# Performance work log

Hardware: AMD Instinct MI355X
Metric: run time of the kernel (lower is better)

The kernel has to match this reference:

```python
import jax, jax.numpy as jnp
import numpy as np


def _linear_interp(t, S):
    """1D linear interpolation along last axis, matching F.interpolate(mode='linear', align_corners=False).
    t: [B, C, L] -> [B, C, S]"""
    L = t.shape[-1]
    src = jnp.clip((jnp.arange(S, dtype=jnp.float32) + 0.5) * (L / S) - 0.5, 0.0, L - 1)
    i0 = jnp.floor(src).astype(jnp.int32)
    i1 = jnp.minimum(i0 + 1, L - 1)
    w = (src - i0.astype(jnp.float32)).astype(t.dtype)
    return t[..., i0] * (1.0 - w) + t[..., i1] * w


def setup_inputs() -> dict:
    key = jax.random.key(0)
    k1, k2, k3, k4 = jax.random.split(key, 4)
    B, C, H, W, L, D = 32, 768, 32, 32, 77, 512
    return {
        "img_feat": jax.random.normal(k1, (B, C, H, W), dtype=jnp.float32),
        "text_feat": jax.random.normal(k2, (B, L, D), dtype=jnp.float32),
        "W_txt": jax.random.normal(k3, (D, C), dtype=jnp.float32) / np.float32(np.sqrt(D)),
        "gamma": jax.random.normal(k4, (1,), dtype=jnp.float32) * 0.1,
    }


def reference(img_feat, text_feat, W_txt, gamma):
    B, C, H, W = img_feat.shape
    S = H * W
    q = img_feat.reshape(B, C, S)                          # [B,C,S]
    # Linear(D->C, bias=False) then transpose(1,2): [B,L,D] -> [B,C,L]
    t = jnp.einsum('bld,dc->bcl', text_feat, W_txt)
    t = _linear_interp(t, S)                               # [B,C,S]
    scale = S ** (-0.5)
    # attn = bmm(q [B,C,S], t^T [B,S,C]) * scale -> [B,C,C] channel attention
    attn = jax.nn.softmax(jnp.einsum('bis,bjs->bij', q, t) * scale, axis=-1)
    out = q + gamma * jnp.einsum('bij,bjs->bis', attn, t)  # gamma-gated residual
    return out.reshape(B, C, H, W)
```

## Files before the change

### kernel.cpp

```cpp
#include <hip/hip_runtime.h>

#define BB 32
#define CC 768
#define SS 1024
#define LLn 77
#define DD 512
#define LP 80
#define LP2 96
#define QBS 264
#define WREG 8448

#define RATIO 0.0751953125f

#define CVT_TXT_BLOCKS (BB * LP * DD / 4 / 256)
#define CVT_W_BLOCKS ((CC / 32) * (DD / 32))
#define AB_BLOCKS (4 * 5 * 8 * 64 * 8 / 4 / 256)
#define TG_BLOCKS (BB * 5 * 4)

typedef short bf16x8 __attribute__((ext_vector_type(8)));
typedef float f32x4 __attribute__((ext_vector_type(4)));
typedef unsigned short u16;

#define MFMA __builtin_amdgcn_mfma_f32_16x16x32_bf16

__device__ __forceinline__ float bf2f(unsigned int h16) {
    unsigned int u = h16 << 16;
    float f; __builtin_memcpy(&f, &u, 4); return f;
}
__device__ __forceinline__ u16 f2bf(float f) {
    unsigned int u; __builtin_memcpy(&u, &f, 4);
    u += 0x7fffu + ((u >> 16) & 1u);
    return (u16)(u >> 16);
}

__global__ __launch_bounds__(256) void k_cvt(const float* __restrict__ text,
                                             const float* __restrict__ Wt,
                                             u16* __restrict__ At,
                                             u16* __restrict__ Wb,
                                             u16* __restrict__ Abf) {
    __shared__ float tile[32 * 33];
    const int bx = blockIdx.x;
    const int tid = threadIdx.x;
    if (bx < CVT_TXT_BLOCKS) {
        int j = bx * 256 + tid;
        int row80 = j >> 7, col4 = (j & 127) << 2;
        int b = row80 / LP, l = row80 - b * LP;
        u16 o[4] = {0, 0, 0, 0};
        if (l < LLn) {
            float4 v = *reinterpret_cast<const float4*>(&text[((size_t)b * LLn + l) * DD + col4]);
            o[0] = f2bf(v.x); o[1] = f2bf(v.y); o[2] = f2bf(v.z); o[3] = f2bf(v.w);
        }
        *reinterpret_cast<uint2*>(&At[(size_t)row80 * DD + col4]) = *reinterpret_cast<uint2*>(o);
    } else if (bx < CVT_TXT_BLOCKS + CVT_W_BLOCKS) {
        const int bw = bx - CVT_TXT_BLOCKS;
        const int c0 = (bw % (CC / 32)) * 32, d0 = (bw / (CC / 32)) * 32;
        const int tx = tid & 31, ty = tid >> 5;
#pragma unroll
        for (int k = 0; k < 4; ++k) {
            int d = ty + k * 8;
            tile[d * 33 + tx] = Wt[(size_t)(d0 + d) * CC + c0 + tx];
        }
        __syncthreads();
#pragma unroll
        for (int k = 0; k < 4; ++k) {
            int c = ty + k * 8;
            Wb[(size_t)(c0 + c) * DD + d0 + tx] = f2bf(tile[tx * 33 + c]);
        }
    } else {
        int g = (bx - CVT_TXT_BLOCKS - CVT_W_BLOCKS) * 1024 + tid * 4;
        int e0   = g & 7;
        int lane = (g >> 3) & 63;
        int kk   = (g >> 9) & 7;
        int nt   = (g >> 12) % 5;
        int w    = g / 20480;
        int l    = nt * 16 + (lane & 15);
        int sb   = w * 256 + kk * 32 + ((lane >> 4) << 3) + e0;
        float fl = (float)l;
        u16 o[4];
#pragma unroll
        for (int k = 0; k < 4; ++k) {
            float src = fmaf((float)(sb + k) + 0.5f, RATIO, -0.5f);
            src = fminf(fmaxf(src, 0.f), 76.f);
            o[k] = f2bf(fmaxf(0.f, 1.f - fabsf(src - fl)) * 0.03125f);
        }
        *reinterpret_cast<uint2*>(&Abf[g]) = *reinterpret_cast<uint2*>(o);
    }
}

__global__ __launch_bounds__(256) void k_tgemm(const u16* __restrict__ At,
                                               const u16* __restrict__ Wb,
                                               u16* __restrict__ tc,
                                               u16* __restrict__ tlc) {
    const int bx = blockIdx.x;
    const int tid = threadIdx.x;
    const int cg = bx / 160, mt = bx % 160;
    const int b = mt / 5, tile = mt % 5;
    const int l0 = tile * 16;
    const int w = tid >> 6, lane = tid & 63;
    const int lm = lane & 15, lg = lane >> 4;
    const int c0 = cg * 192 + w * 48;

    f32x4 acc[3];
#pragma unroll
    for (int nt = 0; nt < 3; ++nt) acc[nt] = (f32x4){0.f, 0.f, 0.f, 0.f};

    const u16* ap = At + ((size_t)b * LP + l0 + lm) * DD + lg * 8;
    const u16* bp = Wb + (size_t)(c0 + lm) * DD + lg * 8;
#pragma unroll 4
    for (int ks = 0; ks < 16; ++ks) {
        bf16x8 aq = *reinterpret_cast<const bf16x8*>(ap + ks * 32);
#pragma unroll
        for (int nt = 0; nt < 3; ++nt) {
            bf16x8 bv = *reinterpret_cast<const bf16x8*>(bp + (size_t)nt * 16 * DD + ks * 32);
            acc[nt] = MFMA(aq, bv, acc[nt], 0, 0, 0);
        }
    }

    const int lq = l0 + lg * 4;
#pragma unroll
    for (int nt = 0; nt < 3; ++nt) {
        int c = c0 + nt * 16 + lm;
        u16 pk[4];
#pragma unroll
        for (int r = 0; r < 4; ++r) pk[r] = f2bf(acc[nt][r]);
        uint2 pv; __builtin_memcpy(&pv, pk, 8);
        *reinterpret_cast<uint2*>(&tc[((size_t)b * CC + c) * LP2 + lq]) = pv;
#pragma unroll
        for (int r = 0; r < 4; ++r)
            tlc[((size_t)b * LP + lq + r) * CC + c] = pk[r];
    }
    if (tile == 4 && lg == 0) {
        uint4 z = {0u, 0u, 0u, 0u};
#pragma unroll
        for (int nt = 0; nt < 3; ++nt) {
            int c = c0 + nt * 16 + lm;
            *reinterpret_cast<uint4*>(&tc[((size_t)b * CC + c) * LP2 + 80]) = z;
            *reinterpret_cast<uint4*>(&tc[((size_t)b * CC + c) * LP2 + 88]) = z;
        }
    }
}

__global__ __launch_bounds__(256, 3) void k_fused(const u16* __restrict__ tc,
                                                  const u16* __restrict__ tlc,
                                                  const u16* __restrict__ Abf,
                                                  const float* __restrict__ q,
                                                  const float* __restrict__ gamma,
                                                  float* __restrict__ out) {
    __shared__ __align__(16) char un[4 * WREG];
    __shared__ __align__(16) char sh2[5120];
    __shared__ float pmax[64];
    __shared__ float psum[64];

    const int id = blockIdx.x;
    const int o = id >> 3;
    const int b = (id & 7) * 4 + o / 48;
    const int iBase = (o % 48) * 16;

    const int tid = threadIdx.x;
    const int w = tid >> 6, lane = tid & 63;
    const int lm = lane & 15, lg = lane >> 4;
    const float g = gamma[0];

    const size_t qBase = ((size_t)b * CC + iBase) * SS + (size_t)(tid << 2);
    const int s0 = tid << 2;
    uint2 qpk[16];
#pragma unroll
    for (int r = 0; r < 16; ++r) {
        f32x4 v = *reinterpret_cast<const f32x4*>(&q[qBase + (size_t)r * SS]);
        u16 pk[4] = {f2bf(v[0]), f2bf(v[1]), f2bf(v[2]), f2bf(v[3])};
        __builtin_memcpy(&qpk[r], pk, 8);
    }
    u16* qbuf = (u16*)(un + w * WREG);
#pragma unroll
    for (int r = 0; r < 16; ++r)
        *reinterpret_cast<uint2*>(&qbuf[r * QBS + lane * 4]) = qpk[r];

    f32x4 aqh[5];
#pragma unroll
    for (int nt = 0; nt < 5; ++nt) aqh[nt] = (f32x4){0.f, 0.f, 0.f, 0.f};
    const u16* abw = Abf + ((size_t)(w * 5) << 12) + (lane << 3);
#pragma unroll
    for (int kk = 0; kk < 8; ++kk) {
        bf16x8 av = *reinterpret_cast<const bf16x8*>(&qbuf[lm * QBS + kk * 32 + lg * 8]);
#pragma unroll
        for (int nt = 0; nt < 5; ++nt) {
            bf16x8 bv = *reinterpret_cast<const bf16x8*>(abw + (((nt << 3) + kk) << 9));
            aqh[nt] = MFMA(av, bv, aqh[nt], 0, 0, 0);
        }
    }
    {
        float* qp = (float*)(un + w * WREG);
#pragma unroll
        for (int nt = 0; nt < 5; ++nt) {
#pragma unroll
            for (int r = 0; r < 4; ++r)
                qp[(lg * 4 + r) * 80 + nt * 16 + lm] = aqh[nt][r];
        }
    }
    __syncthreads();

    u16* qh_bf = (u16*)sh2;
#pragma unroll
    for (int k = 0; k < 5; ++k) {
        int e = tid + (k << 8);
        int row = e / 80, l = e - row * 80;
        float v = ((float*)(un))[row * 80 + l]
                + ((float*)(un + WREG))[row * 80 + l]
                + ((float*)(un + 2 * WREG))[row * 80 + l]
                + ((float*)(un + 3 * WREG))[row * 80 + l];
        qh_bf[row * 96 + l] = f2bf(v);
    }
    if (tid < 16 * 16) qh_bf[(tid >> 4) * 96 + 80 + (tid & 15)] = 0;
    __syncthreads();

    bf16x8 aq0 = *reinterpret_cast<const bf16x8*>(&qh_bf[lm * 96 + lg * 8]);
    bf16x8 aq1 = *reinterpret_cast<const bf16x8*>(&qh_bf[lm * 96 + 32 + lg * 8]);
    bf16x8 aq2 = *reinterpret_cast<const bf16x8*>(&qh_bf[lm * 96 + 64 + lg * 8]);

    f32x4 acc[12];
#pragma unroll
    for (int t = 0; t < 12; ++t) acc[t] = (f32x4){0.f, 0.f, 0.f, 0.f};

    const u16* tcb = tc + ((size_t)b * CC + w * 192 + lm) * LP2 + lg * 8;
#pragma unroll
    for (int t = 0; t < 12; ++t) {
        const u16* p = tcb + (size_t)t * 16 * LP2;
        bf16x8 b0 = *reinterpret_cast<const bf16x8*>(p);
        bf16x8 b1 = *reinterpret_cast<const bf16x8*>(p + 32);
        bf16x8 b2 = *reinterpret_cast<const bf16x8*>(p + 64);
        acc[t] = MFMA(aq0, b0, acc[t], 0, 0, 0);
        acc[t] = MFMA(aq1, b1, acc[t], 0, 0, 0);
        acc[t] = MFMA(aq2, b2, acc[t], 0, 0, 0);
    }

    float m[4];
#pragma unroll
    for (int r = 0; r < 4; ++r) {
        float mm = acc[0][r];
#pragma unroll
        for (int t = 1; t < 12; ++t) mm = fmaxf(mm, acc[t][r]);
#pragma unroll
        for (int off = 8; off >= 1; off >>= 1) mm = fmaxf(mm, __shfl_xor(mm, off));
        m[r] = mm;
    }
    if (lm == 0) {
#pragma unroll
        for (int r = 0; r < 4; ++r) pmax[w * 16 + lg * 4 + r] = m[r];
    }
    __syncthreads();
    float gm[4];
#pragma unroll
    for (int r = 0; r < 4; ++r) {
        int row = lg * 4 + r;
        gm[r] = fmaxf(fmaxf(pmax[row], pmax[16 + row]), fmaxf(pmax[32 + row], pmax[48 + row]));
    }
    float s[4] = {0.f, 0.f, 0.f, 0.f};
#pragma unroll
    for (int t = 0; t < 12; ++t) {
#pragma unroll
        for (int r = 0; r < 4; ++r) {
            float e = __expf(acc[t][r] - gm[r]);
            acc[t][r] = e;
            s[r] += e;
        }
    }
#pragma unroll
    for (int r = 0; r < 4; ++r) {
#pragma unroll
        for (int off = 8; off >= 1; off >>= 1) s[r] += __shfl_xor(s[r], off);
    }
    if (lm == 0) {
#pragma unroll
        for (int r = 0; r < 4; ++r) psum[w * 16 + lg * 4 + r] = s[r];
    }

    u16* P = (u16*)(un + w * WREG);
#pragma unroll
    for (int t = 0; t < 12; ++t) {
#pragma unroll
        for (int r = 0; r < 4; ++r)
            P[(lg * 4 + r) * 200 + t * 16 + lm] = f2bf(acc[t][r]);
    }

    f32x4 u[5];
#pragma unroll
    for (int nt = 0; nt < 5; ++nt) u[nt] = (f32x4){0.f, 0.f, 0.f, 0.f};
    const u16* tb = tlc + ((size_t)b * LP + lm) * CC + w * 192 + lg * 8;
#pragma unroll
    for (int ks = 0; ks < 6; ++ks) {
        bf16x8 pa = *reinterpret_cast<const bf16x8*>(&P[lm * 200 + ks * 32 + lg * 8]);
#pragma unroll
        for (int nt = 0; nt < 5; ++nt) {
            bf16x8 bv = *reinterpret_cast<const bf16x8*>(tb + (size_t)nt * 16 * CC + ks * 32);
            u[nt] = MFMA(pa, bv, u[nt], 0, 0, 0);
        }
    }

    float* up = (float*)(un + w * WREG);
#pragma unroll
    for (int nt = 0; nt < 5; ++nt) {
#pragma unroll
        for (int r = 0; r < 4; ++r)
            up[(lg * 4 + r) * 81 + nt * 16 + lm] = u[nt][r];
    }
    __syncthreads();
    float* us = (float*)sh2;
#pragma unroll
    for (int k = 0; k < 5; ++k) {
        int idx = tid + (k << 8);
        int row = idx / LP, l = idx - row * LP;
        float v = ((float*)(un))[row * 81 + l]
                + ((float*)(un + WREG))[row * 81 + l]
                + ((float*)(un + 2 * WREG))[row * 81 + l]
                + ((float*)(un + 3 * WREG))[row * 81 + l];
        float denom = psum[row] + psum[16 + row] + psum[32 + row] + psum[48 + row];
        us[row * LP + l] = v / denom;
    }
    __syncthreads();

    float wgt[4]; int i0k[4], i1x[4];
#pragma unroll
    for (int k = 0; k < 4; ++k) {
        float src = fmaf((float)(s0 + k) + 0.5f, RATIO, -0.5f);
        src = fminf(fmaxf(src, 0.f), 76.f);
        i0k[k] = (int)src;
        wgt[k] = src - (float)i0k[k];
        i1x[k] = (i0k[k] < 76) ? i0k[k] + 1 : 76;
    }
#pragma unroll
    for (int r = 0; r < 16; ++r) {
        const float* ur = &us[r * LP];
        uint2 qq = qpk[r];
        float qf[4] = {bf2f(qq.x & 0xffffu), bf2f(qq.x >> 16),
                       bf2f(qq.y & 0xffffu), bf2f(qq.y >> 16)};
        f32x4 ov;
#pragma unroll
        for (int k = 0; k < 4; ++k) {
            float uv = fmaf(1.f - wgt[k], ur[i0k[k]], wgt[k] * ur[i1x[k]]);
            ov[k] = qf[k] + g * uv;
        }
        __builtin_nontemporal_store(ov, reinterpret_cast<f32x4*>(&out[qBase + (size_t)r * SS]));
    }
}

extern "C" void kernel_launch(void* const* d_in, const int* in_sizes, int n_in,
                              void* d_out, int out_size, void* d_ws, size_t ws_size,
                              hipStream_t stream) {
    const float* img   = (const float*)d_in[0];
    const float* text  = (const float*)d_in[1];
    const float* Wt    = (const float*)d_in[2];
    const float* gamma = (const float*)d_in[3];
    float* out = (float*)d_out;
    char* ws = (char*)d_ws;
    u16*   tc_bf  = (u16*)(ws);
    u16*   tlc_bf = (u16*)(ws + 4718592);
    u16*   At_bf  = (u16*)(ws + 8650752);
    u16*   Wb_bf  = (u16*)(ws + 11272192);
    u16*   Abf_bf = (u16*)(ws + 12058624);

    k_cvt<<<dim3(CVT_TXT_BLOCKS + CVT_W_BLOCKS + AB_BLOCKS), 256, 0, stream>>>(
        text, Wt, At_bf, Wb_bf, Abf_bf);
    k_tgemm<<<dim3(TG_BLOCKS), 256, 0, stream>>>(At_bf, Wb_bf, tc_bf, tlc_bf);
    k_fused<<<dim3(48 * BB), 256, 0, stream>>>(tc_bf, tlc_bf, Abf_bf, img, gamma, out);
}
```

Baseline: 97.70 us.

## Split fused attention block across eight waves instead of four

The fused kernel moves from 256 to 512 threads per block. Each wave now owns 128 spatial positions and 96 channels instead of 256 and 192. The interpolation matrix layout in the convert kernel is rearranged to match, and the cross-wave reductions now sum eight partials. The aim is more waves in flight per CU to hide latency on the q loads and tc/tlc reads. The cost is narrower global accesses (2-float loads and stores), more LDS reduction work and larger barrier groups.

```diff
diff --git a/kernel.cpp b/kernel.cpp
--- a/kernel.cpp
+++ b/kernel.cpp
@@ -7,19 +7,20 @@
 #define DD 512
 #define LP 80
 #define LP2 96
-#define QBS 264
-#define WREG 8448
+#define WREG2 5184
 
 #define RATIO 0.0751953125f
 
 #define CVT_TXT_BLOCKS (BB * LP * DD / 4 / 256)
 #define CVT_W_BLOCKS ((CC / 32) * (DD / 32))
-#define AB_BLOCKS (4 * 5 * 8 * 64 * 8 / 4 / 256)
+#define AB_BLOCKS (8 * 5 * 4 * 64 * 8 / 4 / 256)
 #define TG_BLOCKS (BB * 5 * 4)
 
 typedef short bf16x8 __attribute__((ext_vector_type(8)));
 typedef float f32x4 __attribute__((ext_vector_type(4)));
+typedef float f32x2 __attribute__((ext_vector_type(2)));
 typedef unsigned short u16;
+typedef unsigned int u32;
 
 #define MFMA __builtin_amdgcn_mfma_f32_16x16x32_bf16
 
@@ -70,11 +71,12 @@
         int g = (bx - CVT_TXT_BLOCKS - CVT_W_BLOCKS) * 1024 + tid * 4;
         int e0   = g & 7;
         int lane = (g >> 3) & 63;
-        int kk   = (g >> 9) & 7;
-        int nt   = (g >> 12) % 5;
-        int w    = g / 20480;
+        int kk   = (g >> 9) & 3;
+        int wn   = g >> 11;
+        int nt   = wn % 5;
+        int wv   = wn / 5;
         int l    = nt * 16 + (lane & 15);
-        int sb   = w * 256 + kk * 32 + ((lane >> 4) << 3) + e0;
+        int sb   = wv * 128 + kk * 32 + ((lane >> 4) << 3) + e0;
         float fl = (float)l;
         u16 o[4];
 #pragma unroll
@@ -140,16 +142,16 @@
     }
 }
 
-__global__ __launch_bounds__(256, 3) void k_fused(const u16* __restrict__ tc,
+__global__ __launch_bounds__(512, 4) void k_fused(const u16* __restrict__ tc,
                                                   const u16* __restrict__ tlc,
                                                   const u16* __restrict__ Abf,
                                                   const float* __restrict__ q,
                                                   const float* __restrict__ gamma,
                                                   float* __restrict__ out) {
-    __shared__ __align__(16) char un[4 * WREG];
+    __shared__ __align__(16) char un[8 * WREG2];
     __shared__ __align__(16) char sh2[5120];
-    __shared__ float pmax[64];
-    __shared__ float psum[64];
+    __shared__ float pmax[128];
+    __shared__ float psum[128];
 
     const int id = blockIdx.x;
     const int o = id >> 3;
@@ -157,39 +159,38 @@
     const int iBase = (o % 48) * 16;
 
     const int tid = threadIdx.x;
-    const int w = tid >> 6, lane = tid & 63;
+    const int wv = tid >> 6, lane = tid & 63;
     const int lm = lane & 15, lg = lane >> 4;
     const float g = gamma[0];
 
-    const size_t qBase = ((size_t)b * CC + iBase) * SS + (size_t)(tid << 2);
-    const int s0 = tid << 2;
-    uint2 qpk[16];
+    const int c0 = wv * 128 + lane * 2;
+    const size_t qRow = ((size_t)b * CC + iBase) * SS + c0;
+    u32 qpk[16];
 #pragma unroll
     for (int r = 0; r < 16; ++r) {
-        f32x4 v = *reinterpret_cast<const f32x4*>(&q[qBase + (size_t)r * SS]);
-        u16 pk[4] = {f2bf(v[0]), f2bf(v[1]), f2bf(v[2]), f2bf(v[3])};
-        __builtin_memcpy(&qpk[r], pk, 8);
-    }
-    u16* qbuf = (u16*)(un + w * WREG);
+        f32x2 v = *reinterpret_cast<const f32x2*>(&q[qRow + (size_t)r * SS]);
+        qpk[r] = (u32)f2bf(v[0]) | ((u32)f2bf(v[1]) << 16);
+    }
+    u16* qbuf = (u16*)(un + wv * WREG2);
 #pragma unroll
     for (int r = 0; r < 16; ++r)
-        *reinterpret_cast<uint2*>(&qbuf[r * QBS + lane * 4]) = qpk[r];
+        *reinterpret_cast<u32*>(&qbuf[r * 136 + lane * 2]) = qpk[r];
 
     f32x4 aqh[5];
 #pragma unroll
     for (int nt = 0; nt < 5; ++nt) aqh[nt] = (f32x4){0.f, 0.f, 0.f, 0.f};
-    const u16* abw = Abf + ((size_t)(w * 5) << 12) + (lane << 3);
-#pragma unroll
-    for (int kk = 0; kk < 8; ++kk) {
-        bf16x8 av = *reinterpret_cast<const bf16x8*>(&qbuf[lm * QBS + kk * 32 + lg * 8]);
+    const u16* abw = Abf + (size_t)wv * 10240 + lane * 8;
+#pragma unroll
+    for (int kk = 0; kk < 4; ++kk) {
+        bf16x8 av = *reinterpret_cast<const bf16x8*>(&qbuf[lm * 136 + kk * 32 + lg * 8]);
 #pragma unroll
         for (int nt = 0; nt < 5; ++nt) {
-            bf16x8 bv = *reinterpret_cast<const bf16x8*>(abw + (((nt << 3) + kk) << 9));
+            bf16x8 bv = *reinterpret_cast<const bf16x8*>(abw + ((nt * 4 + kk) << 9));
             aqh[nt] = MFMA(av, bv, aqh[nt], 0, 0, 0);
         }
     }
     {
-        float* qp = (float*)(un + w * WREG);
+        float* qp = (float*)(un + wv * WREG2);
 #pragma unroll
         for (int nt = 0; nt < 5; ++nt) {
 #pragma unroll
@@ -201,29 +202,30 @@
 
     u16* qh_bf = (u16*)sh2;
 #pragma unroll
-    for (int k = 0; k < 5; ++k) {
-        int e = tid + (k << 8);
-        int row = e / 80, l = e - row * 80;
-        float v = ((float*)(un))[row * 80 + l]
-                + ((float*)(un + WREG))[row * 80 + l]
-                + ((float*)(un + 2 * WREG))[row * 80 + l]
-                + ((float*)(un + 3 * WREG))[row * 80 + l];
-        qh_bf[row * 96 + l] = f2bf(v);
-    }
-    if (tid < 16 * 16) qh_bf[(tid >> 4) * 96 + 80 + (tid & 15)] = 0;
+    for (int k = 0; k < 3; ++k) {
+        int e = tid + (k << 9);
+        if (e < 1280) {
+            int row = e / 80, l = e - row * 80;
+            float v = 0.f;
+#pragma unroll
+            for (int i = 0; i < 8; ++i) v += ((float*)(un + i * WREG2))[row * 80 + l];
+            qh_bf[row * 96 + l] = f2bf(v);
+        }
+    }
+    if (tid < 256) qh_bf[(tid >> 4) * 96 + 80 + (tid & 15)] = 0;
     __syncthreads();
 
     bf16x8 aq0 = *reinterpret_cast<const bf16x8*>(&qh_bf[lm * 96 + lg * 8]);
     bf16x8 aq1 = *reinterpret_cast<const bf16x8*>(&qh_bf[lm * 96 + 32 + lg * 8]);
     bf16x8 aq2 = *reinterpret_cast<const bf16x8*>(&qh_bf[lm * 96 + 64 + lg * 8]);
 
-    f32x4 acc[12];
-#pragma unroll
-    for (int t = 0; t < 12; ++t) acc[t] = (f32x4){0.f, 0.f, 0.f, 0.f};
-
-    const u16* tcb = tc + ((size_t)b * CC + w * 192 + lm) * LP2 + lg * 8;
-#pragma unroll
-    for (int t = 0; t < 12; ++t) {
+    f32x4 acc[6];
+#pragma unroll
+    for (int t = 0; t < 6; ++t) acc[t] = (f32x4){0.f, 0.f, 0.f, 0.f};
+
+    const u16* tcb = tc + ((size_t)b * CC + wv * 96 + lm) * LP2 + lg * 8;
+#pragma unroll
+    for (int t = 0; t < 6; ++t) {
         const u16* p = tcb + (size_t)t * 16 * LP2;
         bf16x8 b0 = *reinterpret_cast<const bf16x8*>(p);
         bf16x8 b1 = *reinterpret_cast<const bf16x8*>(p + 32);
@@ -238,25 +240,29 @@
     for (int r = 0; r < 4; ++r) {
         float mm = acc[0][r];
 #pragma unroll
-        for (int t = 1; t < 12; ++t) mm = fmaxf(mm, acc[t][r]);
+        for (int t = 1; t < 6; ++t) mm = fmaxf(mm, acc[t][r]);
 #pragma unroll
         for (int off = 8; off >= 1; off >>= 1) mm = fmaxf(mm, __shfl_xor(mm, off));
         m[r] = mm;
     }
     if (lm == 0) {
 #pragma unroll
-        for (int r = 0; r < 4; ++r) pmax[w * 16 + lg * 4 + r] = m[r];
+        for (int r = 0; r < 4; ++r) pmax[wv * 16 + lg * 4 + r] = m[r];
     }
     __syncthreads();
     float gm[4];
 #pragma unroll
     for (int r = 0; r < 4; ++r) {
         int row = lg * 4 + r;
-        gm[r] = fmaxf(fmaxf(pmax[row], pmax[16 + row]), fmaxf(pmax[32 + row], pmax[48 + row]));
+        float a01 = fmaxf(pmax[row], pmax[16 + row]);
+        float a23 = fmaxf(pmax[32 + row], pmax[48 + row]);
+        float a45 = fmaxf(pmax[64 + row], pmax[80 + row]);
+        float a67 = fmaxf(pmax[96 + row], pmax[112 + row]);
+        gm[r] = fmaxf(fmaxf(a01, a23), fmaxf(a45, a67));
     }
     float s[4] = {0.f, 0.f, 0.f, 0.f};
 #pragma unroll
-    for (int t = 0; t < 12; ++t) {
+    for (int t = 0; t < 6; ++t) {
 #pragma unroll
         for (int r = 0; r < 4; ++r) {
             float e = __expf(acc[t][r] - gm[r]);
@@ -271,24 +277,24 @@
     }
     if (lm == 0) {
 #pragma unroll
-        for (int r = 0; r < 4; ++r) psum[w * 16 + lg * 4 + r] = s[r];
-    }
-
-    u16* P = (u16*)(un + w * WREG);
-#pragma unroll
-    for (int t = 0; t < 12; ++t) {
+        for (int r = 0; r < 4; ++r) psum[wv * 16 + lg * 4 + r] = s[r];
+    }
+
+    u16* P = (u16*)(un + wv * WREG2);
+#pragma unroll
+    for (int t = 0; t < 6; ++t) {
 #pragma unroll
         for (int r = 0; r < 4; ++r)
-            P[(lg * 4 + r) * 200 + t * 16 + lm] = f2bf(acc[t][r]);
+            P[(lg * 4 + r) * 104 + t * 16 + lm] = f2bf(acc[t][r]);
     }
 
     f32x4 u[5];
 #pragma unroll
     for (int nt = 0; nt < 5; ++nt) u[nt] = (f32x4){0.f, 0.f, 0.f, 0.f};
-    const u16* tb = tlc + ((size_t)b * LP + lm) * CC + w * 192 + lg * 8;
-#pragma unroll
-    for (int ks = 0; ks < 6; ++ks) {
-        bf16x8 pa = *reinterpret_cast<const bf16x8*>(&P[lm * 200 + ks * 32 + lg * 8]);
+    const u16* tb = tlc + ((size_t)b * LP + lm) * CC + wv * 96 + lg * 8;
+#pragma unroll
+    for (int ks = 0; ks < 3; ++ks) {
+        bf16x8 pa = *reinterpret_cast<const bf16x8*>(&P[lm * 104 + ks * 32 + lg * 8]);
 #pragma unroll
         for (int nt = 0; nt < 5; ++nt) {
             bf16x8 bv = *reinterpret_cast<const bf16x8*>(tb + (size_t)nt * 16 * CC + ks * 32);
@@ -296,7 +302,7 @@
         }
     }
 
-    float* up = (float*)(un + w * WREG);
+    float* up = (float*)(un + wv * WREG2);
 #pragma unroll
     for (int nt = 0; nt < 5; ++nt) {
 #pragma unroll
@@ -306,40 +312,37 @@
     __syncthreads();
     float* us = (float*)sh2;
 #pragma unroll
-    for (int k = 0; k < 5; ++k) {
-        int idx = tid + (k << 8);
-        int row = idx / LP, l = idx - row * LP;
-        float v = ((float*)(un))[row * 81 + l]
-                + ((float*)(un + WREG))[row * 81 + l]
-                + ((float*)(un + 2 * WREG))[row * 81 + l]
-                + ((float*)(un + 3 * WREG))[row * 81 + l];
-        float denom = psum[row] + psum[16 + row] + psum[32 + row] + psum[48 + row];
-        us[row * LP + l] = v / denom;
-    }
-    __syncthreads();
-
-    float wgt[4]; int i0k[4], i1x[4];
-#pragma unroll
-    for (int k = 0; k < 4; ++k) {
-        float src = fmaf((float)(s0 + k) + 0.5f, RATIO, -0.5f);
-        src = fminf(fmaxf(src, 0.f), 76.f);
-        i0k[k] = (int)src;
-        wgt[k] = src - (float)i0k[k];
-        i1x[k] = (i0k[k] < 76) ? i0k[k] + 1 : 76;
-    }
+    for (int k = 0; k < 3; ++k) {
+        int e = tid + (k << 9);
+        if (e < 1280) {
+            int row = e / 80, l = e - row * 80;
+            float v = 0.f;
+#pragma unroll
+            for (int i = 0; i < 8; ++i) v += ((float*)(un + i * WREG2))[row * 81 + l];
+            float denom = 0.f;
+#pragma unroll
+            for (int i = 0; i < 8; ++i) denom += psum[i * 16 + row];
+            us[row * 80 + l] = v / denom;
+        }
+    }
+    __syncthreads();
+
+    float srcA = fminf(fmaxf(fmaf((float)c0 + 0.5f, RATIO, -0.5f), 0.f), 76.f);
+    float srcB = fminf(fmaxf(fmaf((float)c0 + 1.5f, RATIO, -0.5f), 0.f), 76.f);
+    int i0a = (int)srcA, i0b = (int)srcB;
+    float wa = srcA - (float)i0a, wb = srcB - (float)i0b;
+    int i1a = (i0a < 76) ? i0a + 1 : 76;
+    int i1b = (i0b < 76) ? i0b + 1 : 76;
 #pragma unroll
     for (int r = 0; r < 16; ++r) {
-        const float* ur = &us[r * LP];
-        uint2 qq = qpk[r];
-        float qf[4] = {bf2f(qq.x & 0xffffu), bf2f(qq.x >> 16),
-                       bf2f(qq.y & 0xffffu), bf2f(qq.y >> 16)};
-        f32x4 ov;
-#pragma unroll
-        for (int k = 0; k < 4; ++k) {
-            float uv = fmaf(1.f - wgt[k], ur[i0k[k]], wgt[k] * ur[i1x[k]]);
-            ov[k] = qf[k] + g * uv;
-        }
-        __builtin_nontemporal_store(ov, reinterpret_cast<f32x4*>(&out[qBase + (size_t)r * SS]));
+        const float* ur = &us[r * 80];
+        float ua = fmaf(1.f - wa, ur[i0a], wa * ur[i1a]);
+        float ub = fmaf(1.f - wb, ur[i0b], wb * ur[i1b]);
+        u32 qq = qpk[r];
+        f32x2 ov;
+        ov[0] = bf2f(qq & 0xffffu) + g * ua;
+        ov[1] = bf2f(qq >> 16) + g * ub;
+        __builtin_nontemporal_store(ov, reinterpret_cast<f32x2*>(&out[qRow + (size_t)r * SS]));
     }
 }
 
@@ -361,5 +364,5 @@
     k_cvt<<<dim3(CVT_TXT_BLOCKS + CVT_W_BLOCKS + AB_BLOCKS), 256, 0, stream>>>(
         text, Wt, At_bf, Wb_bf, Abf_bf);
     k_tgemm<<<dim3(TG_BLOCKS), 256, 0, stream>>>(At_bf, Wb_bf, tc_bf, tlc_bf);
-    k_fused<<<dim3(48 * BB), 256, 0, stream>>>(tc_bf, tlc_bf, Abf_bf, img, gamma, out);
-}
+    k_fused<<<dim3(48 * BB), 512, 0, stream>>>(tc_bf, tlc_bf, Abf_bf, img, gamma, out);
+}
```

New measurement: 101.8 us. 4.2% more time.

## Split q-projection into the text GEMM kernel and reload q in fp32 for output

Applied to the files above, without the earlier changes.

The q·A interpolation projection (qh) moves out of the fused attention kernel into a combined middle kernel of 512-thread blocks that also runs the text GEMM. qh is written to global memory in bf16. The attention kernel then only reads qh, runs softmax and the second GEMM, and re-reads q in fp32 for the residual instead of keeping bf16 copies. The aim is to raise occupancy and overlap the two middle-stage workloads, and the fp32 residual also improves accuracy. In exchange q is read from HBM twice and qh takes an extra global round trip.

```diff
diff --git a/kernel.cpp b/kernel.cpp
--- a/kernel.cpp
+++ b/kernel.cpp
@@ -7,19 +7,21 @@
 #define DD 512
 #define LP 80
 #define LP2 96
-#define QBS 264
-#define WREG 8448
+#define WREG2 5184
 
 #define RATIO 0.0751953125f
 
 #define CVT_TXT_BLOCKS (BB * LP * DD / 4 / 256)
 #define CVT_W_BLOCKS ((CC / 32) * (DD / 32))
-#define AB_BLOCKS (4 * 5 * 8 * 64 * 8 / 4 / 256)
-#define TG_BLOCKS (BB * 5 * 4)
+#define AB_BLOCKS (8 * 5 * 4 * 64 * 8 / 4 / 256)
+#define QH_BLOCKS (48 * BB)
+#define TG2_BLOCKS (BB * 5 * 2)
 
 typedef short bf16x8 __attribute__((ext_vector_type(8)));
 typedef float f32x4 __attribute__((ext_vector_type(4)));
+typedef float f32x2 __attribute__((ext_vector_type(2)));
 typedef unsigned short u16;
+typedef unsigned int u32;
 
 #define MFMA __builtin_amdgcn_mfma_f32_16x16x32_bf16
 
@@ -70,11 +72,12 @@
         int g = (bx - CVT_TXT_BLOCKS - CVT_W_BLOCKS) * 1024 + tid * 4;
         int e0   = g & 7;
         int lane = (g >> 3) & 63;
-        int kk   = (g >> 9) & 7;
-        int nt   = (g >> 12) % 5;
-        int w    = g / 20480;
+        int kk   = (g >> 9) & 3;
+        int wn   = g >> 11;
+        int nt   = wn % 5;
+        int wv   = wn / 5;
         int l    = nt * 16 + (lane & 15);
-        int sb   = w * 256 + kk * 32 + ((lane >> 4) << 3) + e0;
+        int sb   = wv * 128 + kk * 32 + ((lane >> 4) << 3) + e0;
         float fl = (float)l;
         u16 o[4];
 #pragma unroll
@@ -87,135 +90,146 @@
     }
 }
 
-__global__ __launch_bounds__(256) void k_tgemm(const u16* __restrict__ At,
-                                               const u16* __restrict__ Wb,
-                                               u16* __restrict__ tc,
-                                               u16* __restrict__ tlc) {
+__global__ __launch_bounds__(512, 2) void k_mid2(const float* __restrict__ q,
+                                                 const u16* __restrict__ Abf,
+                                                 const u16* __restrict__ At,
+                                                 const u16* __restrict__ Wb,
+                                                 u16* __restrict__ qh,
+                                                 u16* __restrict__ tc,
+                                                 u16* __restrict__ tlc) {
+    __shared__ __align__(16) char un[8 * WREG2];
     const int bx = blockIdx.x;
     const int tid = threadIdx.x;
-    const int cg = bx / 160, mt = bx % 160;
-    const int b = mt / 5, tile = mt % 5;
-    const int l0 = tile * 16;
-    const int w = tid >> 6, lane = tid & 63;
+    const int wv = tid >> 6, lane = tid & 63;
     const int lm = lane & 15, lg = lane >> 4;
-    const int c0 = cg * 192 + w * 48;
-
-    f32x4 acc[3];
-#pragma unroll
-    for (int nt = 0; nt < 3; ++nt) acc[nt] = (f32x4){0.f, 0.f, 0.f, 0.f};
-
-    const u16* ap = At + ((size_t)b * LP + l0 + lm) * DD + lg * 8;
-    const u16* bp = Wb + (size_t)(c0 + lm) * DD + lg * 8;
+
+    if (bx < QH_BLOCKS) {
+        const int o = bx >> 3;
+        const int b = (bx & 7) * 4 + o / 48;
+        const int iBase = (o % 48) * 16;
+
+        const int c0 = wv * 128 + lane * 2;
+        const size_t qRow = ((size_t)b * CC + iBase) * SS + c0;
+        u32 qpk[16];
+#pragma unroll
+        for (int r = 0; r < 16; ++r) {
+            f32x2 v = *reinterpret_cast<const f32x2*>(&q[qRow + (size_t)r * SS]);
+            qpk[r] = (u32)f2bf(v[0]) | ((u32)f2bf(v[1]) << 16);
+        }
+        u16* qbuf = (u16*)(un + wv * WREG2);
+#pragma unroll
+        for (int r = 0; r < 16; ++r)
+            *reinterpret_cast<u32*>(&qbuf[r * 136 + lane * 2]) = qpk[r];
+
+        f32x4 aqh[5];
+#pragma unroll
+        for (int nt = 0; nt < 5; ++nt) aqh[nt] = (f32x4){0.f, 0.f, 0.f, 0.f};
+        const u16* abw = Abf + (size_t)wv * 10240 + lane * 8;
+#pragma unroll
+        for (int kk = 0; kk < 4; ++kk) {
+            bf16x8 av = *reinterpret_cast<const bf16x8*>(&qbuf[lm * 136 + kk * 32 + lg * 8]);
+#pragma unroll
+            for (int nt = 0; nt < 5; ++nt) {
+                bf16x8 bv = *reinterpret_cast<const bf16x8*>(abw + ((nt * 4 + kk) << 9));
+                aqh[nt] = MFMA(av, bv, aqh[nt], 0, 0, 0);
+            }
+        }
+        {
+            float* qp = (float*)(un + wv * WREG2);
+#pragma unroll
+            for (int nt = 0; nt < 5; ++nt) {
+#pragma unroll
+                for (int r = 0; r < 4; ++r)
+                    qp[(lg * 4 + r) * 80 + nt * 16 + lm] = aqh[nt][r];
+            }
+        }
+        __syncthreads();
+
+        for (int e2 = tid; e2 < 16 * 48; e2 += 512) {
+            int row = e2 / 48, j = e2 - row * 48;
+            int l0 = 2 * j;
+            float v0 = 0.f, v1 = 0.f;
+            if (l0 < 80) {
+#pragma unroll
+                for (int i = 0; i < 8; ++i) v0 += ((float*)(un + i * WREG2))[row * 80 + l0];
+#pragma unroll
+                for (int i = 0; i < 8; ++i) v1 += ((float*)(un + i * WREG2))[row * 80 + l0 + 1];
+            }
+            u32 pk = (u32)f2bf(v0) | ((u32)f2bf(v1) << 16);
+            *reinterpret_cast<u32*>(&qh[((size_t)b * CC + iBase + row) * LP2 + l0]) = pk;
+        }
+    } else {
+        const int bt = bx - QH_BLOCKS;
+        const int cg = bt / 160, mt = bt % 160;
+        const int b = mt / 5, tile = mt % 5;
+        const int l0 = tile * 16;
+        const int c0 = cg * 384 + wv * 48;
+
+        f32x4 acc[3];
+#pragma unroll
+        for (int nt = 0; nt < 3; ++nt) acc[nt] = (f32x4){0.f, 0.f, 0.f, 0.f};
+
+        const u16* ap = At + ((size_t)b * LP + l0 + lm) * DD + lg * 8;
+        const u16* bp = Wb + (size_t)(c0 + lm) * DD + lg * 8;
 #pragma unroll 4
-    for (int ks = 0; ks < 16; ++ks) {
-        bf16x8 aq = *reinterpret_cast<const bf16x8*>(ap + ks * 32);
-#pragma unroll
-        for (int nt = 0; nt < 3; ++nt) {
-            bf16x8 bv = *reinterpret_cast<const bf16x8*>(bp + (size_t)nt * 16 * DD + ks * 32);
-            acc[nt] = MFMA(aq, bv, acc[nt], 0, 0, 0);
-        }
-    }
-
-    const int lq = l0 + lg * 4;
-#pragma unroll
-    for (int nt = 0; nt < 3; ++nt) {
-        int c = c0 + nt * 16 + lm;
-        u16 pk[4];
-#pragma unroll
-        for (int r = 0; r < 4; ++r) pk[r] = f2bf(acc[nt][r]);
-        uint2 pv; __builtin_memcpy(&pv, pk, 8);
-        *reinterpret_cast<uint2*>(&tc[((size_t)b * CC + c) * LP2 + lq]) = pv;
-#pragma unroll
-        for (int r = 0; r < 4; ++r)
-            tlc[((size_t)b * LP + lq + r) * CC + c] = pk[r];
-    }
-    if (tile == 4 && lg == 0) {
-        uint4 z = {0u, 0u, 0u, 0u};
+        for (int ks = 0; ks < 16; ++ks) {
+            bf16x8 aq = *reinterpret_cast<const bf16x8*>(ap + ks * 32);
+#pragma unroll
+            for (int nt = 0; nt < 3; ++nt) {
+                bf16x8 bv = *reinterpret_cast<const bf16x8*>(bp + (size_t)nt * 16 * DD + ks * 32);
+                acc[nt] = MFMA(aq, bv, acc[nt], 0, 0, 0);
+            }
+        }
+
+        const int lq = l0 + lg * 4;
 #pragma unroll
         for (int nt = 0; nt < 3; ++nt) {
             int c = c0 + nt * 16 + lm;
-            *reinterpret_cast<uint4*>(&tc[((size_t)b * CC + c) * LP2 + 80]) = z;
-            *reinterpret_cast<uint4*>(&tc[((size_t)b * CC + c) * LP2 + 88]) = z;
-        }
-    }
-}
-
-__global__ __launch_bounds__(256, 3) void k_fused(const u16* __restrict__ tc,
-                                                  const u16* __restrict__ tlc,
-                                                  const u16* __restrict__ Abf,
-                                                  const float* __restrict__ q,
-                                                  const float* __restrict__ gamma,
-                                                  float* __restrict__ out) {
-    __shared__ __align__(16) char un[4 * WREG];
-    __shared__ __align__(16) char sh2[5120];
-    __shared__ float pmax[64];
-    __shared__ float psum[64];
+            u16 pk[4];
+#pragma unroll
+            for (int r = 0; r < 4; ++r) pk[r] = f2bf(acc[nt][r]);
+            uint2 pv; __builtin_memcpy(&pv, pk, 8);
+            *reinterpret_cast<uint2*>(&tc[((size_t)b * CC + c) * LP2 + lq]) = pv;
+#pragma unroll
+            for (int r = 0; r < 4; ++r)
+                tlc[((size_t)b * LP + lq + r) * CC + c] = pk[r];
+        }
+        if (tile == 4 && lg == 0) {
+            uint4 z = {0u, 0u, 0u, 0u};
+#pragma unroll
+            for (int nt = 0; nt < 3; ++nt) {
+                int c = c0 + nt * 16 + lm;
+                *reinterpret_cast<uint4*>(&tc[((size_t)b * CC + c) * LP2 + 80]) = z;
+                *reinterpret_cast<uint4*>(&tc[((size_t)b * CC + c) * LP2 + 88]) = z;
+            }
+        }
+    }
+}
+
+__global__ __launch_bounds__(256, 2) void k_attn_out(const u16* __restrict__ qh,
+                                                     const u16* __restrict__ tc,
+                                                     const u16* __restrict__ tlc,
+                                                     const float* __restrict__ q,
+                                                     const float* __restrict__ gamma,
+                                                     float* __restrict__ out) {
+    __shared__ float pmax[4][16];
+    __shared__ float psum[4][16];
+    __shared__ float us[16 * 80];
+    __shared__ __align__(16) char pbuf[4][6400];
 
     const int id = blockIdx.x;
     const int o = id >> 3;
     const int b = (id & 7) * 4 + o / 48;
     const int iBase = (o % 48) * 16;
-
     const int tid = threadIdx.x;
     const int w = tid >> 6, lane = tid & 63;
     const int lm = lane & 15, lg = lane >> 4;
     const float g = gamma[0];
 
-    const size_t qBase = ((size_t)b * CC + iBase) * SS + (size_t)(tid << 2);
-    const int s0 = tid << 2;
-    uint2 qpk[16];
-#pragma unroll
-    for (int r = 0; r < 16; ++r) {
-        f32x4 v = *reinterpret_cast<const f32x4*>(&q[qBase + (size_t)r * SS]);
-        u16 pk[4] = {f2bf(v[0]), f2bf(v[1]), f2bf(v[2]), f2bf(v[3])};
-        __builtin_memcpy(&qpk[r], pk, 8);
-    }
-    u16* qbuf = (u16*)(un + w * WREG);
-#pragma unroll
-    for (int r = 0; r < 16; ++r)
-        *reinterpret_cast<uint2*>(&qbuf[r * QBS + lane * 4]) = qpk[r];
-
-    f32x4 aqh[5];
-#pragma unroll
-    for (int nt = 0; nt < 5; ++nt) aqh[nt] = (f32x4){0.f, 0.f, 0.f, 0.f};
-    const u16* abw = Abf + ((size_t)(w * 5) << 12) + (lane << 3);
-#pragma unroll
-    for (int kk = 0; kk < 8; ++kk) {
-        bf16x8 av = *reinterpret_cast<const bf16x8*>(&qbuf[lm * QBS + kk * 32 + lg * 8]);
-#pragma unroll
-        for (int nt = 0; nt < 5; ++nt) {
-            bf16x8 bv = *reinterpret_cast<const bf16x8*>(abw + (((nt << 3) + kk) << 9));
-            aqh[nt] = MFMA(av, bv, aqh[nt], 0, 0, 0);
-        }
-    }
-    {
-        float* qp = (float*)(un + w * WREG);
-#pragma unroll
-        for (int nt = 0; nt < 5; ++nt) {
-#pragma unroll
-            for (int r = 0; r < 4; ++r)
-                qp[(lg * 4 + r) * 80 + nt * 16 + lm] = aqh[nt][r];
-        }
-    }
-    __syncthreads();
-
-    u16* qh_bf = (u16*)sh2;
-#pragma unroll
-    for (int k = 0; k < 5; ++k) {
-        int e = tid + (k << 8);
-        int row = e / 80, l = e - row * 80;
-        float v = ((float*)(un))[row * 80 + l]
-                + ((float*)(un + WREG))[row * 80 + l]
-                + ((float*)(un + 2 * WREG))[row * 80 + l]
-                + ((float*)(un + 3 * WREG))[row * 80 + l];
-        qh_bf[row * 96 + l] = f2bf(v);
-    }
-    if (tid < 16 * 16) qh_bf[(tid >> 4) * 96 + 80 + (tid & 15)] = 0;
-    __syncthreads();
-
-    bf16x8 aq0 = *reinterpret_cast<const bf16x8*>(&qh_bf[lm * 96 + lg * 8]);
-    bf16x8 aq1 = *reinterpret_cast<const bf16x8*>(&qh_bf[lm * 96 + 32 + lg * 8]);
-    bf16x8 aq2 = *reinterpret_cast<const bf16x8*>(&qh_bf[lm * 96 + 64 + lg * 8]);
+    const u16* qbase = qh + ((size_t)b * CC + iBase + lm) * LP2 + lg * 8;
+    bf16x8 aq0 = *reinterpret_cast<const bf16x8*>(qbase);
+    bf16x8 aq1 = *reinterpret_cast<const bf16x8*>(qbase + 32);
+    bf16x8 aq2 = *reinterpret_cast<const bf16x8*>(qbase + 64);
 
     f32x4 acc[12];
 #pragma unroll
@@ -233,6 +247,12 @@
         acc[t] = MFMA(aq2, b2, acc[t], 0, 0, 0);
     }
 
+    const size_t qBase = ((size_t)b * CC + iBase) * SS + (size_t)(tid << 2);
+    f32x4 qreg[16];
+#pragma unroll
+    for (int r = 0; r < 16; ++r)
+        qreg[r] = *reinterpret_cast<const f32x4*>(&q[qBase + (size_t)r * SS]);
+
     float m[4];
 #pragma unroll
     for (int r = 0; r < 4; ++r) {
@@ -245,14 +265,14 @@
     }
     if (lm == 0) {
 #pragma unroll
-        for (int r = 0; r < 4; ++r) pmax[w * 16 + lg * 4 + r] = m[r];
+        for (int r = 0; r < 4; ++r) pmax[w][lg * 4 + r] = m[r];
     }
     __syncthreads();
     float gm[4];
 #pragma unroll
     for (int r = 0; r < 4; ++r) {
         int row = lg * 4 + r;
-        gm[r] = fmaxf(fmaxf(pmax[row], pmax[16 + row]), fmaxf(pmax[32 + row], pmax[48 + row]));
+        gm[r] = fmaxf(fmaxf(pmax[0][row], pmax[1][row]), fmaxf(pmax[2][row], pmax[3][row]));
     }
     float s[4] = {0.f, 0.f, 0.f, 0.f};
 #pragma unroll
@@ -271,10 +291,10 @@
     }
     if (lm == 0) {
 #pragma unroll
-        for (int r = 0; r < 4; ++r) psum[w * 16 + lg * 4 + r] = s[r];
-    }
-
-    u16* P = (u16*)(un + w * WREG);
+        for (int r = 0; r < 4; ++r) psum[w][lg * 4 + r] = s[r];
+    }
+
+    u16* P = (u16*)pbuf[w];
 #pragma unroll
     for (int t = 0; t < 12; ++t) {
 #pragma unroll
@@ -296,7 +316,7 @@
         }
     }
 
-    float* up = (float*)(un + w * WREG);
+    float* up = (float*)pbuf[w];
 #pragma unroll
     for (int nt = 0; nt < 5; ++nt) {
 #pragma unroll
@@ -304,20 +324,18 @@
             up[(lg * 4 + r) * 81 + nt * 16 + lm] = u[nt][r];
     }
     __syncthreads();
-    float* us = (float*)sh2;
 #pragma unroll
     for (int k = 0; k < 5; ++k) {
         int idx = tid + (k << 8);
         int row = idx / LP, l = idx - row * LP;
-        float v = ((float*)(un))[row * 81 + l]
-                + ((float*)(un + WREG))[row * 81 + l]
-                + ((float*)(un + 2 * WREG))[row * 81 + l]
-                + ((float*)(un + 3 * WREG))[row * 81 + l];
-        float denom = psum[row] + psum[16 + row] + psum[32 + row] + psum[48 + row];
+        float v = ((float*)pbuf[0])[row * 81 + l] + ((float*)pbuf[1])[row * 81 + l]
+                + ((float*)pbuf[2])[row * 81 + l] + ((float*)pbuf[3])[row * 81 + l];
+        float denom = psum[0][row] + psum[1][row] + psum[2][row] + psum[3][row];
         us[row * LP + l] = v / denom;
     }
     __syncthreads();
 
+    const int s0 = tid << 2;
     float wgt[4]; int i0k[4], i1x[4];
 #pragma unroll
     for (int k = 0; k < 4; ++k) {
@@ -330,14 +348,11 @@
 #pragma unroll
     for (int r = 0; r < 16; ++r) {
         const float* ur = &us[r * LP];
-        uint2 qq = qpk[r];
-        float qf[4] = {bf2f(qq.x & 0xffffu), bf2f(qq.x >> 16),
-                       bf2f(qq.y & 0xffffu), bf2f(qq.y >> 16)};
         f32x4 ov;
 #pragma unroll
         for (int k = 0; k < 4; ++k) {
             float uv = fmaf(1.f - wgt[k], ur[i0k[k]], wgt[k] * ur[i1x[k]]);
-            ov[k] = qf[k] + g * uv;
+            ov[k] = qreg[r][k] + g * uv;
         }
         __builtin_nontemporal_store(ov, reinterpret_cast<f32x4*>(&out[qBase + (size_t)r * SS]));
     }
@@ -354,12 +369,14 @@
     char* ws = (char*)d_ws;
     u16*   tc_bf  = (u16*)(ws);
     u16*   tlc_bf = (u16*)(ws + 4718592);
-    u16*   At_bf  = (u16*)(ws + 8650752);
-    u16*   Wb_bf  = (u16*)(ws + 11272192);
-    u16*   Abf_bf = (u16*)(ws + 12058624);
+    u16*   qh_bf  = (u16*)(ws + 8650752);
+    u16*   At_bf  = (u16*)(ws + 13369344);
+    u16*   Wb_bf  = (u16*)(ws + 15990784);
+    u16*   Abf_bf = (u16*)(ws + 16777216);
 
     k_cvt<<<dim3(CVT_TXT_BLOCKS + CVT_W_BLOCKS + AB_BLOCKS), 256, 0, stream>>>(
         text, Wt, At_bf, Wb_bf, Abf_bf);
-    k_tgemm<<<dim3(TG_BLOCKS), 256, 0, stream>>>(At_bf, Wb_bf, tc_bf, tlc_bf);
-    k_fused<<<dim3(48 * BB), 256, 0, stream>>>(tc_bf, tlc_bf, Abf_bf, img, gamma, out);
-}
+    k_mid2<<<dim3(QH_BLOCKS + TG2_BLOCKS), 512, 0, stream>>>(
+        img, Abf_bf, At_bf, Wb_bf, qh_bf, tc_bf, tlc_bf);
+    k_attn_out<<<dim3(QH_BLOCKS), 256, 0, stream>>>(qh_bf, tc_bf, tlc_bf, img, gamma, out);
+}
```

Measured after the change: 108.7 us. 11.2% more time.
